# Optimization experiments

Measured on AMD Instinct MI355X. Metric: run time of the kernel, lower is better.

The kernel has to match this reference:

```python
import jax, jax.numpy as jnp
import numpy as np

EMBED_DIM = 1024
NUM_HEADS = 16
HEAD_DIM = EMBED_DIM // NUM_HEADS


def setup_inputs() -> dict:
    key = jax.random.key(0)
    ks = jax.random.split(key, 6)
    s = 1.0 / np.sqrt(EMBED_DIM)
    x = jax.random.normal(ks[0], (2, 2048, EMBED_DIM), dtype=jnp.float32)
    Wk = jax.random.uniform(ks[1], (EMBED_DIM, EMBED_DIM), jnp.float32, -s, s)
    Wq = jax.random.uniform(ks[2], (EMBED_DIM, EMBED_DIM), jnp.float32, -s, s)
    Wv = jax.random.uniform(ks[3], (EMBED_DIM, EMBED_DIM), jnp.float32, -s, s)
    Wo = jax.random.uniform(ks[4], (EMBED_DIM, EMBED_DIM), jnp.float32, -s, s)
    bo = jax.random.uniform(ks[5], (EMBED_DIM,), jnp.float32, -s, s)
    return {"x": x, "Wq": Wq, "Wk": Wk, "Wv": Wv, "Wo": Wo, "bo": bo}


def reference(x, Wq, Wk, Wv, Wo, bo):
    b, s, e = x.shape
    h, d = NUM_HEADS, HEAD_DIM
    scale = d ** (-0.5)
    # nn.Linear: y = x @ W.T ; here W stored as [out, in] -> use W.T
    q = (x @ Wq.T).reshape(b, s, h, d).transpose(0, 2, 1, 3)  # b h s d
    k = (x @ Wk.T).reshape(b, s, h, d).transpose(0, 2, 1, 3)
    v = (x @ Wv.T).reshape(b, s, h, d).transpose(0, 2, 1, 3)
    logits = jnp.einsum('bhqd,bhkd->bhqk', q, k) * scale
    attn = jax.nn.softmax(logits, axis=-1)
    out = jnp.einsum('bhqk,bhkd->bhqd', attn, v)
    out = out.transpose(0, 2, 1, 3).reshape(b, s, e)
    return out @ Wo.T + bo
```

## Files before the change

kernel.cpp:

```cpp
#include <hip/hip_runtime.h>
#include <hip/hip_bf16.h>

using short8 = __attribute__((ext_vector_type(8))) short;
using f32x4  = __attribute__((ext_vector_type(4))) float;
using uint4v = __attribute__((ext_vector_type(4))) unsigned;

#if __has_builtin(__builtin_amdgcn_exp2f)
#define EXP2(x) __builtin_amdgcn_exp2f(x)
#else
#define EXP2(x) exp2f(x)
#endif

__device__ __forceinline__ short f2bf(float f) {
    union { float f; unsigned u; } v; v.f = f;
    unsigned r = v.u + 0x7fffu + ((v.u >> 16) & 1u);
    return (short)(r >> 16);
}
__device__ __forceinline__ unsigned pack_trunc(float a, float b) {
    union { float f; unsigned u; } ua, ub; ua.f = a; ub.f = b;
#if __has_builtin(__builtin_amdgcn_perm)
    return __builtin_amdgcn_perm(ub.u, ua.u, 0x07060302u);
#else
    return (ub.u & 0xFFFF0000u) | (ua.u >> 16);
#endif
}
__device__ __forceinline__ void async_copy16(const short* g, short* s) {
    __builtin_amdgcn_global_load_lds(
        (const __attribute__((address_space(1))) void*)g,
        (__attribute__((address_space(3))) void*)s, 16, 0, 0);
}

__global__ __launch_bounds__(256) void cvt_f32_bf16(
    const float* __restrict__ s0, const float* __restrict__ s1,
    const float* __restrict__ s2, const float* __restrict__ s3,
    const float* __restrict__ s4,
    short* __restrict__ d0, short* __restrict__ d1, short* __restrict__ d2,
    short* __restrict__ d3, short* __restrict__ d4) {
    const int bid = blockIdx.x;
    const float* s; short* d; int base;
    if (bid < 4096) {
        s = s0; d = d0; base = bid << 10;
    } else {
        const int r = bid - 4096;
        base = (r & 1023) << 10;
        switch (r >> 10) {
            case 0: s = s1; d = d1; break;
            case 1: s = s2; d = d2; break;
            case 2: s = s3; d = d3; break;
            default: s = s4; d = d4; break;
        }
    }
    const int idx = base + threadIdx.x * 4;
    float4 v = *(const float4*)(s + idx);
    short4 o;
    o.x = f2bf(v.x); o.y = f2bf(v.y); o.z = f2bf(v.z); o.w = f2bf(v.w);
    *(short4*)(d + idx) = o;
}

template <int MODE>
__device__ __forceinline__ void gemm_body(const short* __restrict__ A,
                                          const short* __restrict__ B,
                                          short* __restrict__ C,
                                          float scale,
                                          short* __restrict__ As,
                                          short* __restrict__ Bs) {
    constexpr int Kd = 1024, Nd = 1024, Sd = 2048;

    const int tid  = threadIdx.x;
    const int w    = tid >> 6, lane = tid & 63;
    const int quad = lane >> 4, l16 = lane & 15;
    const int xr   = l16 & 7;
    const int wm   = (w >> 1) * 64, wn = (w & 1) * 64;
    const int bm   = blockIdx.y * 128, bn = blockIdx.x * 128;

    f32x4 acc[4][4];
#pragma unroll
    for (int i = 0; i < 4; ++i)
#pragma unroll
        for (int j = 0; j < 4; ++j) acc[i][j] = (f32x4){0.f, 0.f, 0.f, 0.f};

    for (int k0 = 0; k0 < Kd; k0 += 64) {
        __syncthreads();
#pragma unroll
        for (int c = 0; c < 4; ++c) {
            int li   = c * 256 + tid;
            int row  = li >> 3;
            int gcol = ((li & 7) ^ (row & 7)) * 8;
            async_copy16(A + (size_t)(bm + row) * Kd + k0 + gcol, &As[li * 8]);
            async_copy16(B + (size_t)(bn + row) * Kd + k0 + gcol, &Bs[li * 8]);
        }
        __syncthreads();

#pragma unroll
        for (int kk = 0; kk < 2; ++kk) {
            short8 af[4], bfv[4];
#pragma unroll
            for (int mi = 0; mi < 4; ++mi) {
                const int r = wm + mi * 16 + l16;
                af[mi] = *(const short8*)(
                    &As[r * 64 + (((kk * 4 + quad) ^ xr) * 8)]);
            }
#pragma unroll
            for (int ni = 0; ni < 4; ++ni) {
                const int r = wn + ni * 16 + l16;
                bfv[ni] = *(const short8*)(
                    &Bs[r * 64 + (((kk * 4 + quad) ^ xr) * 8)]);
            }
#pragma unroll
            for (int mi = 0; mi < 4; ++mi)
#pragma unroll
                for (int ni = 0; ni < 4; ++ni) {
                    if constexpr (MODE == 2)
                        acc[mi][ni] = __builtin_amdgcn_mfma_f32_16x16x32_bf16(
                            bfv[ni], af[mi], acc[mi][ni], 0, 0, 0);
                    else
                        acc[mi][ni] = __builtin_amdgcn_mfma_f32_16x16x32_bf16(
                            af[mi], bfv[ni], acc[mi][ni], 0, 0, 0);
                }
        }
    }

    if constexpr (MODE == 2) {
#pragma unroll
        for (int mi = 0; mi < 4; ++mi) {
            const int m_g = bm + wm + mi * 16 + l16;
            const int b_  = m_g >> 11, s_ = m_g & 2047;
#pragma unroll
            for (int ni = 0; ni < 4; ++ni)
#pragma unroll
                for (int r = 0; r < 4; ++r) {
                    const int n_g = bn + wn + ni * 16 + quad * 4 + r;
                    C[(size_t)b_ * Nd * Sd + (size_t)n_g * Sd + s_] =
                        f2bf(acc[mi][ni][r]);
                }
        }
    } else {
#pragma unroll
        for (int ni = 0; ni < 4; ++ni) {
            const int colg = bn + wn + ni * 16 + l16;
#pragma unroll
            for (int mi = 0; mi < 4; ++mi)
#pragma unroll
                for (int r = 0; r < 4; ++r) {
                    const int rowg = bm + wm + mi * 16 + quad * 4 + r;
                    C[(size_t)rowg * Nd + colg] = f2bf(acc[mi][ni][r] * scale);
                }
        }
    }
}

#define CSC 0.18033688f

__global__ __launch_bounds__(256, 3) void proj_gemm(
    const short* __restrict__ X,
    const short* __restrict__ Wq, const short* __restrict__ Wk,
    const short* __restrict__ Wv,
    short* __restrict__ Qo, short* __restrict__ Ko, short* __restrict__ VTo) {
    __shared__ __align__(16) short As[128 * 64];
    __shared__ __align__(16) short Bs[128 * 64];
    if (blockIdx.z == 0)
        gemm_body<0>(X, Wq, Qo, CSC, As, Bs);
    else if (blockIdx.z == 1)
        gemm_body<0>(X, Wk, Ko, 1.0f, As, Bs);
    else
        gemm_body<2>(X, Wv, VTo, 1.0f, As, Bs);
}

__global__ __launch_bounds__(256, 2) void out_gemm(
    const short* __restrict__ A, const short* __restrict__ B,
    const float* __restrict__ bias, float* __restrict__ C) {
    constexpr int Kd = 1024, Nd = 1024;
    __shared__ __align__(16) short As[64 * 64];
    __shared__ __align__(16) short Bs[128 * 64];

    const int tid  = threadIdx.x;
    const int w    = tid >> 6, lane = tid & 63;
    const int quad = lane >> 4, l16 = lane & 15;
    const int xr   = l16 & 7;
    const int wm   = (w >> 1) * 32, wn = (w & 1) * 64;
    const int bm   = blockIdx.y * 64, bn = blockIdx.x * 128;

    f32x4 acc[2][4];
#pragma unroll
    for (int i = 0; i < 2; ++i)
#pragma unroll
        for (int j = 0; j < 4; ++j) acc[i][j] = (f32x4){0.f, 0.f, 0.f, 0.f};

    for (int k0 = 0; k0 < Kd; k0 += 64) {
        __syncthreads();
#pragma unroll
        for (int c = 0; c < 2; ++c) {
            int li   = c * 256 + tid;
            int row  = li >> 3;
            int gcol = ((li & 7) ^ (row & 7)) * 8;
            async_copy16(A + (size_t)(bm + row) * Kd + k0 + gcol, &As[li * 8]);
        }
#pragma unroll
        for (int c = 0; c < 4; ++c) {
            int li   = c * 256 + tid;
            int row  = li >> 3;
            int gcol = ((li & 7) ^ (row & 7)) * 8;
            async_copy16(B + (size_t)(bn + row) * Kd + k0 + gcol, &Bs[li * 8]);
        }
        __syncthreads();

#pragma unroll
        for (int kk = 0; kk < 2; ++kk) {
            short8 af[2], bfv[4];
#pragma unroll
            for (int mi = 0; mi < 2; ++mi) {
                const int r = wm + mi * 16 + l16;
                af[mi] = *(const short8*)(
                    &As[r * 64 + (((kk * 4 + quad) ^ xr) * 8)]);
            }
#pragma unroll
            for (int ni = 0; ni < 4; ++ni) {
                const int r = wn + ni * 16 + l16;
                bfv[ni] = *(const short8*)(
                    &Bs[r * 64 + (((kk * 4 + quad) ^ xr) * 8)]);
            }
#pragma unroll
            for (int mi = 0; mi < 2; ++mi)
#pragma unroll
                for (int ni = 0; ni < 4; ++ni)
                    acc[mi][ni] = __builtin_amdgcn_mfma_f32_16x16x32_bf16(
                        af[mi], bfv[ni], acc[mi][ni], 0, 0, 0);
        }
    }

#pragma unroll
    for (int ni = 0; ni < 4; ++ni) {
        const int colg = bn + wn + ni * 16 + l16;
        const float bv = bias[colg];
#pragma unroll
        for (int mi = 0; mi < 2; ++mi)
#pragma unroll
            for (int r = 0; r < 4; ++r) {
                const int rowg = bm + wm + mi * 16 + quad * 4 + r;
                C[(size_t)rowg * Nd + colg] = acc[mi][ni][r] + bv;
            }
    }
}

__global__ __launch_bounds__(256, 2) void attn_kernel(
    const short* __restrict__ Q, const short* __restrict__ K,
    const short* __restrict__ VT, short* __restrict__ O) {
    constexpr int S = 2048, E = 1024, KV = 128, NT = S / KV;
    __shared__ __align__(16) short Ks[2][KV * 64];
    __shared__ __align__(16) short Vs[2][64 * KV];

    const int tid  = threadIdx.x;
    const int w    = tid >> 6, lane = tid & 63;
    const int quad = lane >> 4, l16 = lane & 15;

    const int bid  = blockIdx.x;
    const int xcd  = bid & 7, slot = bid >> 3;
    const int qt   = slot & 15;
    const int bh   = xcd + ((slot >> 4) << 3);
    const int b    = bh >> 4, h = bh & 15;

    const int    q0   = qt * 128 + w * 32;
    const size_t base = (size_t)b * S * E;
    const size_t vtb  = (size_t)b * E * S;
    const int    hc   = h * 64;
    const int    xr   = l16 & 7;

    short8 aq[2][2];
#pragma unroll
    for (int qg = 0; qg < 2; ++qg) {
        const short* qp = Q + base + (size_t)(q0 + qg * 16 + l16) * E + hc + quad * 8;
        aq[qg][0] = *(const short8*)(qp);
        aq[qg][1] = *(const short8*)(qp + 32);
    }

    f32x4 oT[2][4], o_sum[2];
#pragma unroll
    for (int qg = 0; qg < 2; ++qg) {
        o_sum[qg] = (f32x4){0.f, 0.f, 0.f, 0.f};
#pragma unroll
        for (int i = 0; i < 4; ++i) oT[qg][i] = (f32x4){0.f, 0.f, 0.f, 0.f};
    }

    int          kdst[4], vdst0[4], vdst1[4];
    const short* kga[4];
    const short* vga[4];
#pragma unroll
    for (int c = 0; c < 4; ++c) {
        const int li = c * 256 + tid;
        {
            const int row = li >> 3, cc = li & 7;
            kdst[c] = row * 64 + ((cc ^ (row & 7)) * 8);
            kga[c]  = K + base + (size_t)row * E + hc + cc * 8;
        }
        {
            const int row = li >> 4, cc = li & 15;
            const int c0   = 4 * (cc >> 2) + 2 * (cc & 1);
            const int boff = 4 * ((cc >> 1) & 1);
            vdst0[c] = row * KV + (((c0)     ^ (row & 7)) * 8) + boff;
            vdst1[c] = row * KV + (((c0 + 1) ^ (row & 7)) * 8) + boff;
            vga[c]   = VT + vtb + (size_t)(hc + row) * S + cc * 8;
        }
    }

    short8 kr[4], vr[4];
    auto load_regs = [&](int t) {
#pragma unroll
        for (int c = 0; c < 4; ++c) {
            kr[c] = *(const short8*)(kga[c] + (size_t)t * KV * E);
            vr[c] = *(const short8*)(vga[c] + t * KV);
        }
    };
    auto store_regs = [&](short* Kn, short* Vn) {
#pragma unroll
        for (int c = 0; c < 4; ++c) {
            *(short8*)(&Kn[kdst[c]]) = kr[c];
            short4 lo, hi;
            lo.x = vr[c][0]; lo.y = vr[c][1]; lo.z = vr[c][2]; lo.w = vr[c][3];
            hi.x = vr[c][4]; hi.y = vr[c][5]; hi.z = vr[c][6]; hi.w = vr[c][7];
            *(short4*)(&Vn[vdst0[c]]) = lo;
            *(short4*)(&Vn[vdst1[c]]) = hi;
        }
    };

    const short8 ones = (short8){0x3F80, 0x3F80, 0x3F80, 0x3F80,
                                 0x3F80, 0x3F80, 0x3F80, 0x3F80};
    const float  LB   = 0.00281502f;

    auto compute_tile = [&](const short* Kc, const short* Vc) {
        __builtin_amdgcn_s_setprio(1);
#pragma unroll
        for (int ks = 0; ks < 4; ++ks) {
            uint4v pkq[2];
#pragma unroll
            for (int kh = 0; kh < 2; ++kh) {
                const int    kn  = ks * 2 + kh;
                const short* kb  = &Kc[(kn * 16 + l16) * 64];
                short8       bk0 = *(const short8*)(kb + ((quad ^ xr) * 8));
                short8       bk1 = *(const short8*)(kb + (((quad + 4) ^ xr) * 8));
#pragma unroll
                for (int qg = 0; qg < 2; ++qg) {
                    f32x4 a = (f32x4){LB, LB, LB, LB};
                    a = __builtin_amdgcn_mfma_f32_16x16x32_bf16(bk0, aq[qg][0], a, 0, 0, 0);
                    a = __builtin_amdgcn_mfma_f32_16x16x32_bf16(bk1, aq[qg][1], a, 0, 0, 0);
                    pkq[qg][kh * 2]     = pack_trunc(EXP2(a[0]), EXP2(a[1]));
                    pkq[qg][kh * 2 + 1] = pack_trunc(EXP2(a[2]), EXP2(a[3]));
                }
            }
            short8 pf[2];
#pragma unroll
            for (int qg = 0; qg < 2; ++qg) {
                union { uint4v u; short8 s; } cv;
                cv.u   = pkq[qg];
                pf[qg] = cv.s;
                o_sum[qg] = __builtin_amdgcn_mfma_f32_16x16x32_bf16(
                    ones, pf[qg], o_sum[qg], 0, 0, 0);
            }
#pragma unroll
            for (int ni = 0; ni < 4; ++ni) {
                const int rv = ni * 16 + l16;
                short8 vb = *(const short8*)(
                    &Vc[rv * KV + (((ks * 4 + quad) ^ xr) * 8)]);
#pragma unroll
                for (int qg = 0; qg < 2; ++qg)
                    oT[qg][ni] = __builtin_amdgcn_mfma_f32_16x16x32_bf16(
                        vb, pf[qg], oT[qg][ni], 0, 0, 0);
            }
        }
        __builtin_amdgcn_s_setprio(0);
    };

    load_regs(0);
    store_regs(Ks[0], Vs[0]);
    load_regs(1);
    __syncthreads();

#pragma unroll 1
    for (int kt = 0; kt < NT; ++kt) {
        const int cur = kt & 1;
        if (kt + 1 < NT) {
            store_regs(Ks[cur ^ 1], Vs[cur ^ 1]);
            if (kt + 2 < NT) load_regs(kt + 2);
        }
        compute_tile(Ks[cur], Vs[cur]);
        __syncthreads();
    }

#pragma unroll
    for (int qg = 0; qg < 2; ++qg) {
        const float inv = 1.0f / o_sum[qg][0];
        const int   qg_ = q0 + qg * 16 + l16;
#pragma unroll
        for (int ni = 0; ni < 4; ++ni) {
            short4 ov;
            ov.x = f2bf(oT[qg][ni][0] * inv);
            ov.y = f2bf(oT[qg][ni][1] * inv);
            ov.z = f2bf(oT[qg][ni][2] * inv);
            ov.w = f2bf(oT[qg][ni][3] * inv);
            *(short4*)(&O[base + (size_t)qg_ * E + hc + ni * 16 + quad * 4]) = ov;
        }
    }
}

extern "C" void kernel_launch(void* const* d_in, const int* in_sizes, int n_in,
                              void* d_out, int out_size, void* d_ws, size_t ws_size,
                              hipStream_t stream) {
    const float* x  = (const float*)d_in[0];
    const float* Wq = (const float*)d_in[1];
    const float* Wk = (const float*)d_in[2];
    const float* Wv = (const float*)d_in[3];
    const float* Wo = (const float*)d_in[4];
    const float* bo = (const float*)d_in[5];
    float* out = (float*)d_out;

    constexpr int XN = 2 * 2048 * 1024;
    constexpr int WN = 1024 * 1024;

    short* Xb  = (short*)d_ws;
    short* Wqb = Xb + XN;
    short* Wkb = Wqb + WN;
    short* Wvb = Wkb + WN;
    short* Wob = Wvb + WN;
    short* Qb  = Wob + WN;
    short* Kb  = Qb + XN;
    short* VTb = Kb + XN;

    cvt_f32_bf16<<<dim3(8192), 256, 0, stream>>>(
        x, Wq, Wk, Wv, Wo, Xb, Wqb, Wkb, Wvb, Wob);
    proj_gemm<<<dim3(8, 32, 3), 256, 0, stream>>>(Xb, Wqb, Wkb, Wvb, Qb, Kb, VTb);
    attn_kernel<<<dim3(512), 256, 0, stream>>>(Qb, Kb, VTb, Xb );
    out_gemm<<<dim3(8, 64), 256, 0, stream>>>(Xb, Wob, bo, out);
}
```

Measured before the change: 173.3 us.

## Shrink attention blocks to 2 waves with 64-key tiles and more blocks

The attention kernel now uses 128-thread blocks (2 waves, 64 query rows) instead of 256 threads, and KV tiles of 64 keys instead of 128. The grid doubles to 1024 blocks and the LDS footprint per block drops by half, so more blocks can be resident per CU. The QK exp stage for all four key groups is computed before the PV MFMAs. In exchange, each K/V tile is reused by fewer query rows, which doubles global K/V traffic per query, and the loop now runs twice as many iterations with their syncs.

```diff
diff --git a/kernel.cpp b/kernel.cpp
--- a/kernel.cpp
+++ b/kernel.cpp
@@ -242,12 +242,12 @@
     }
 }
 
-__global__ __launch_bounds__(256, 2) void attn_kernel(
+__global__ __launch_bounds__(128, 4) void attn_kernel(
     const short* __restrict__ Q, const short* __restrict__ K,
     const short* __restrict__ VT, short* __restrict__ O) {
-    constexpr int S = 2048, E = 1024, KV = 128, NT = S / KV;
-    __shared__ __align__(16) short Ks[2][KV * 64];
-    __shared__ __align__(16) short Vs[2][64 * KV];
+    constexpr int S = 2048, E = 1024, NT = S / 64;
+    __shared__ __align__(16) short Ks[2][64 * 64];
+    __shared__ __align__(16) short Vs[2][64 * 64];
 
     const int tid  = threadIdx.x;
     const int w    = tid >> 6, lane = tid & 63;
@@ -255,11 +255,11 @@
 
     const int bid  = blockIdx.x;
     const int xcd  = bid & 7, slot = bid >> 3;
-    const int qt   = slot & 15;
-    const int bh   = xcd + ((slot >> 4) << 3);
+    const int qt   = slot & 31;
+    const int bh   = xcd + ((slot >> 5) << 3);
     const int b    = bh >> 4, h = bh & 15;
 
-    const int    q0   = qt * 128 + w * 32;
+    const int    q0   = qt * 64 + w * 32;
     const size_t base = (size_t)b * S * E;
     const size_t vtb  = (size_t)b * E * S;
     const int    hc   = h * 64;
@@ -286,28 +286,22 @@
     const short* vga[4];
 #pragma unroll
     for (int c = 0; c < 4; ++c) {
-        const int li = c * 256 + tid;
-        {
-            const int row = li >> 3, cc = li & 7;
-            kdst[c] = row * 64 + ((cc ^ (row & 7)) * 8);
-            kga[c]  = K + base + (size_t)row * E + hc + cc * 8;
-        }
-        {
-            const int row = li >> 4, cc = li & 15;
-            const int c0   = 4 * (cc >> 2) + 2 * (cc & 1);
-            const int boff = 4 * ((cc >> 1) & 1);
-            vdst0[c] = row * KV + (((c0)     ^ (row & 7)) * 8) + boff;
-            vdst1[c] = row * KV + (((c0 + 1) ^ (row & 7)) * 8) + boff;
-            vga[c]   = VT + vtb + (size_t)(hc + row) * S + cc * 8;
-        }
+        const int li = c * 128 + tid, row = li >> 3, cc = li & 7;
+        kdst[c] = row * 64 + ((cc ^ (row & 7)) * 8);
+        kga[c]  = K + base + (size_t)row * E + hc + cc * 8;
+        const int c0   = 4 * (cc >> 2) + 2 * (cc & 1);
+        const int boff = 4 * ((cc >> 1) & 1);
+        vdst0[c] = row * 64 + (((c0)     ^ (row & 7)) * 8) + boff;
+        vdst1[c] = row * 64 + (((c0 + 1) ^ (row & 7)) * 8) + boff;
+        vga[c]   = VT + vtb + (size_t)(hc + row) * S + cc * 8;
     }
 
     short8 kr[4], vr[4];
     auto load_regs = [&](int t) {
 #pragma unroll
         for (int c = 0; c < 4; ++c) {
-            kr[c] = *(const short8*)(kga[c] + (size_t)t * KV * E);
-            vr[c] = *(const short8*)(vga[c] + t * KV);
+            kr[c] = *(const short8*)(kga[c] + (size_t)t * 64 * E);
+            vr[c] = *(const short8*)(vga[c] + t * 64);
         }
     };
     auto store_regs = [&](short* Kn, short* Vn) {
@@ -328,29 +322,29 @@
 
     auto compute_tile = [&](const short* Kc, const short* Vc) {
         __builtin_amdgcn_s_setprio(1);
-#pragma unroll
-        for (int ks = 0; ks < 4; ++ks) {
-            uint4v pkq[2];
-#pragma unroll
-            for (int kh = 0; kh < 2; ++kh) {
-                const int    kn  = ks * 2 + kh;
-                const short* kb  = &Kc[(kn * 16 + l16) * 64];
-                short8       bk0 = *(const short8*)(kb + ((quad ^ xr) * 8));
-                short8       bk1 = *(const short8*)(kb + (((quad + 4) ^ xr) * 8));
-#pragma unroll
-                for (int qg = 0; qg < 2; ++qg) {
-                    f32x4 a = (f32x4){LB, LB, LB, LB};
-                    a = __builtin_amdgcn_mfma_f32_16x16x32_bf16(bk0, aq[qg][0], a, 0, 0, 0);
-                    a = __builtin_amdgcn_mfma_f32_16x16x32_bf16(bk1, aq[qg][1], a, 0, 0, 0);
-                    pkq[qg][kh * 2]     = pack_trunc(EXP2(a[0]), EXP2(a[1]));
-                    pkq[qg][kh * 2 + 1] = pack_trunc(EXP2(a[2]), EXP2(a[3]));
-                }
-            }
+        uint4v pkv[2][2];
+#pragma unroll
+        for (int kn = 0; kn < 4; ++kn) {
+            const short* kb  = &Kc[(kn * 16 + l16) * 64];
+            short8       bk0 = *(const short8*)(kb + ((quad ^ xr) * 8));
+            short8       bk1 = *(const short8*)(kb + (((quad + 4) ^ xr) * 8));
+#pragma unroll
+            for (int qg = 0; qg < 2; ++qg) {
+                f32x4 a = (f32x4){LB, LB, LB, LB};
+                a = __builtin_amdgcn_mfma_f32_16x16x32_bf16(bk0, aq[qg][0], a, 0, 0, 0);
+                a = __builtin_amdgcn_mfma_f32_16x16x32_bf16(bk1, aq[qg][1], a, 0, 0, 0);
+                pkv[qg][kn >> 1][(kn & 1) * 2]     = pack_trunc(EXP2(a[0]), EXP2(a[1]));
+                pkv[qg][kn >> 1][(kn & 1) * 2 + 1] = pack_trunc(EXP2(a[2]), EXP2(a[3]));
+            }
+        }
+
+#pragma unroll
+        for (int ks = 0; ks < 2; ++ks) {
             short8 pf[2];
 #pragma unroll
             for (int qg = 0; qg < 2; ++qg) {
                 union { uint4v u; short8 s; } cv;
-                cv.u   = pkq[qg];
+                cv.u   = pkv[qg][ks];
                 pf[qg] = cv.s;
                 o_sum[qg] = __builtin_amdgcn_mfma_f32_16x16x32_bf16(
                     ones, pf[qg], o_sum[qg], 0, 0, 0);
@@ -358,8 +352,8 @@
 #pragma unroll
             for (int ni = 0; ni < 4; ++ni) {
                 const int rv = ni * 16 + l16;
-                short8 vb = *(const short8*)(
-                    &Vc[rv * KV + (((ks * 4 + quad) ^ xr) * 8)]);
+                short8 vb =
+                    *(const short8*)(&Vc[rv * 64 + (((ks * 4 + quad) ^ xr) * 8)]);
 #pragma unroll
                 for (int qg = 0; qg < 2; ++qg)
                     oT[qg][ni] = __builtin_amdgcn_mfma_f32_16x16x32_bf16(
@@ -427,6 +421,6 @@
     cvt_f32_bf16<<<dim3(8192), 256, 0, stream>>>(
         x, Wq, Wk, Wv, Wo, Xb, Wqb, Wkb, Wvb, Wob);
     proj_gemm<<<dim3(8, 32, 3), 256, 0, stream>>>(Xb, Wqb, Wkb, Wvb, Qb, Kb, VTb);
-    attn_kernel<<<dim3(512), 256, 0, stream>>>(Qb, Kb, VTb, Xb );
+    attn_kernel<<<dim3(1024), 128, 0, stream>>>(Qb, Kb, VTb, Xb );
     out_gemm<<<dim3(8, 64), 256, 0, stream>>>(Xb, Wob, bo, out);
 }
```

New measurement: 177.1 us. 2.2% more time.
